# Kernel optimization log

Measured on AMD Instinct MI355X. Metric: run time of the kernel, lower is better.

Reference implementation:

```python
import jax, jax.numpy as jnp
import numpy as np
from jax import lax

T, B, C = 16, 16, 256          # TIMESTEPS, BATCH_SIZE, corr channels
HS, HT = 31, 15                 # search / target feature spatial; VALID corr -> 17x17
OUT = HS - HT + 1               # 17


def setup_inputs() -> dict:
    key = jax.random.key(0)
    k1, k2, k3 = jax.random.split(key, 3)
    s_f = jax.random.normal(k1, (T * B, C, HS, HS), dtype=jnp.float32)
    t_f = jax.random.normal(k2, (B, C, HT, HT), dtype=jnp.float32)
    pos_list = jax.random.randint(k3, (B, T, 2), 0, OUT, dtype=jnp.int32)
    return {"s_f": s_f, "t_f": t_f, "pos_list": pos_list}


def _depthwise_corr(s_b, t_b):
    # s_b: (T, C, 31, 31) search feats for one batch element across timesteps
    # t_b: (C, 15, 15) its target kernel; depthwise cross-correlation per channel
    k = t_b[:, None]  # (C, 1, 15, 15) OIHW with O=C, I=1
    return lax.conv_general_dilated(
        s_b, k, window_strides=(1, 1), padding='VALID',
        dimension_numbers=('NCHW', 'OIHW', 'NCHW'),
        feature_group_count=C)  # (T, C, 17, 17)


def reference(s_f, t_f, pos_list):
    # Correlation_func: torch loops over T doing grouped conv2d; fused here.
    s = s_f.reshape(T, B, C, HS, HS).transpose(1, 0, 2, 3, 4)  # (B, T, C, 31, 31)
    corr = jax.vmap(_depthwise_corr)(s, t_f)                   # (B, T, C, 17, 17)
    # forward(): corr_feat.reshape(T,B,256,17,17).permute(1,0,3,4,2) -> (B,T,17,17,C)
    feat = corr.transpose(0, 1, 3, 4, 2)
    # Chiose_RoW: nested per-element gather -> single advanced-index gather
    bi = jnp.arange(B)[:, None]   # (B, 1)
    ti = jnp.arange(T)[None, :]   # (1, T)
    masks_feat = feat[bi, ti, pos_list[..., 0], pos_list[..., 1]]  # (B, T, C)
    return corr, masks_feat
```

## Files before the change

### kernel.cpp

```cpp
#include <hip/hip_runtime.h>
#include <stdint.h>

#define TT 16
#define BB 16
#define CC 256
#define HS 31
#define HT 15
#define OUTW 17
#define NCH 15
#define NCHAN (BB*TT*CC)
#define CORR_ELEMS ((size_t)NCHAN*OUTW*OUTW)
#define SROW 20
#define SCH  620

typedef _Float16 h2_t __attribute__((ext_vector_type(2)));

__device__ __forceinline__ unsigned packh2(float a, float b) {
    return __builtin_bit_cast(unsigned, __builtin_amdgcn_cvt_pkrtz(a, b));
}
__device__ __forceinline__ float fdot2f(unsigned a, unsigned b, float c) {
    return __builtin_amdgcn_fdot2(__builtin_bit_cast(h2_t, a),
                                  __builtin_bit_cast(h2_t, b), c, false);
}

__device__ __forceinline__ int s_index(int ch) {
    int bt = ch >> 8, c = ch & 255;
    int b = bt >> 4, t = bt & 15;
    return (t * BB + b) * CC + c;
}

__global__ __launch_bounds__(256, 1)
void corr_kernel(const float* __restrict__ s_f, const float* __restrict__ t_f,
                 const int* __restrict__ pos,
                 float* __restrict__ corr, float* __restrict__ masks)
{
    __shared__ unsigned lds[NCH * SCH];

    const int tid = threadIdx.x;
    const int ch_base = blockIdx.x * NCH;

    {
        const int jcol = tid & 15;
        const int r0   = tid >> 4;
        const int x0   = 2 * jcol;
        const bool hasb  = (jcol < 15);
        const int  r1    = r0 + 16;
        const bool hasr1 = (r1 <= 30);
        const int xa = hasb ? x0 : x0 - 1;

        float2 La[NCH], Lb[NCH];
#pragma unroll
        for (int j = 0; j < NCH; ++j) {
            int ch = ch_base + j; if (ch >= NCHAN) ch = NCHAN - 1;
            const float* src = s_f + (size_t)s_index(ch) * (HS * HS);
            La[j] = *(const float2*)(src + r0 * HS + xa);
            Lb[j] = hasr1 ? *(const float2*)(src + r1 * HS + xa)
                          : make_float2(0.f, 0.f);
        }
#pragma unroll
        for (int j = 0; j < NCH; ++j) {
            float a0 = hasb ? La[j].x : La[j].y;
            float b0 = hasb ? La[j].y : 0.0f;
            lds[j * SCH + r0 * SROW + jcol] = packh2(a0, b0);
            if (hasr1) {
                float a1 = hasb ? Lb[j].x : Lb[j].y;
                float b1 = hasb ? Lb[j].y : 0.0f;
                lds[j * SCH + r1 * SROW + jcol] = packh2(a1, b1);
            }
        }
    }

    {
        float2 Lw[8];
        int    off[8];
#pragma unroll
        for (int it = 0; it < 8; ++it) {
            int idx = tid + 256 * it;
            bool ok = idx < NCH * HT * 8;
            int i2  = ok ? idx : 0;
            int j   = i2 / (HT * 8);
            int e   = i2 - j * (HT * 8);
            int ky  = e >> 3, p = e & 7;
            int ch  = ch_base + j; if (ch >= NCHAN) ch = NCHAN - 1;
            int bt = ch >> 8, c = ch & 255, b = bt >> 4;
            const float* wsrc = t_f + (size_t)(b * CC + c) * (HT * HT) + ky * HT;
            int xw = (p < 7) ? 2 * p : 13;
            Lw[it] = *(const float2*)(wsrc + xw);
            off[it] = ok ? (j * SCH + 40 * ky + 16 + ((p & 4) ? 20 + (p & 3) : (p & 3)))
                         : -1;
            if (p == 7) { Lw[it].x = Lw[it].y; Lw[it].y = 0.0f; }
        }
#pragma unroll
        for (int it = 0; it < 8; ++it)
            if (off[it] >= 0) lds[off[it]] = packh2(Lw[it].x, Lw[it].y);
    }

    __syncthreads();

    const int c_sub = tid / OUTW;
    const int oy    = tid - c_sub * OUTW;
    if (c_sub >= NCH) return;
    const int ch = ch_base + c_sub;
    if (ch >= NCHAN) return;

    const unsigned* chb = lds + c_sub * SCH;

    float acc[OUTW];
#pragma unroll
    for (int m = 0; m < OUTW; ++m) acc[m] = 0.0f;

    uint4 A0, A1, A2, A3, AW0, AW1;
    uint4 B0, B1, B2, B3, BW0, BW1;

#define LOADS(S0,S1,S2,S3,W0,W1,KY) do {                                   \
        const uint4* sr = (const uint4*)(chb + (oy + (KY)) * SROW);        \
        S0 = sr[0]; S1 = sr[1]; S2 = sr[2]; S3 = sr[3];                    \
        W0 = *(const uint4*)(chb + 40 * (KY) + 16);                        \
        W1 = *(const uint4*)(chb + 40 * (KY) + 36);                        \
    } while (0)

#define COMPUTE(S0,S1,S2,S3,W0,W1) do {                                    \
        unsigned sp[16] = {S0.x,S0.y,S0.z,S0.w, S1.x,S1.y,S1.z,S1.w,       \
                           S2.x,S2.y,S2.z,S2.w, S3.x,S3.y,S3.z,S3.w};      \
        unsigned wp[8]  = {W0.x,W0.y,W0.z,W0.w, W1.x,W1.y,W1.z,W1.w};      \
        unsigned wo_[8];                                                   \
        wo_[0] = wp[0] << 16;                                              \
        _Pragma("unroll")                                                  \
        for (int r = 1; r < 8; ++r)                                        \
            wo_[r] = __builtin_amdgcn_alignbit(wp[r], wp[r - 1], 16);      \
        _Pragma("unroll")                                                  \
        for (int e = 0; e < 9; ++e)                                        \
            _Pragma("unroll")                                              \
            for (int jj = 0; jj < 8; ++jj)                                 \
                acc[2 * e] = fdot2f(sp[e + jj], wp[jj], acc[2 * e]);       \
        _Pragma("unroll")                                                  \
        for (int o = 0; o < 8; ++o)                                        \
            _Pragma("unroll")                                              \
            for (int r = 0; r < 8; ++r)                                    \
                acc[2 * o + 1] = fdot2f(sp[o + r], wo_[r], acc[2 * o + 1]);\
    } while (0)

    LOADS(A0,A1,A2,A3,AW0,AW1, 0);
#pragma unroll 1
    for (int kk = 0; kk < 7; ++kk) {
        LOADS(B0,B1,B2,B3,BW0,BW1, 2 * kk + 1);
        COMPUTE(A0,A1,A2,A3,AW0,AW1);
        LOADS(A0,A1,A2,A3,AW0,AW1, 2 * kk + 2);
        COMPUTE(B0,B1,B2,B3,BW0,BW1);
    }
    COMPUTE(A0,A1,A2,A3,AW0,AW1);

#undef LOADS
#undef COMPUTE

    float* outp = corr + (size_t)ch * (OUTW * OUTW) + (size_t)oy * OUTW;
#pragma unroll
    for (int m = 0; m < OUTW; ++m) outp[m] = acc[m];

    const int bt = ch >> 8;
    const int p0 = pos[2 * bt];
    const int p1 = pos[2 * bt + 1];
    if (oy == p0) {
        float v = acc[0];
#pragma unroll
        for (int m = 1; m < OUTW; ++m) v = (p1 == m) ? acc[m] : v;
        masks[ch] = v;
    }
}

extern "C" void kernel_launch(void* const* d_in, const int* in_sizes, int n_in,
                              void* d_out, int out_size, void* d_ws, size_t ws_size,
                              hipStream_t stream)
{
    const float* s_f = (const float*)d_in[0];
    const float* t_f = (const float*)d_in[1];
    const int*   pos = (const int*)d_in[2];
    float* corr  = (float*)d_out;
    float* masks = corr + CORR_ELEMS;

    int nblocks = (NCHAN + NCH - 1) / NCH;
    corr_kernel<<<nblocks, 256, 0, stream>>>(s_f, t_f, pos, corr, masks);
}
```

Baseline: 124.8 us.

## Switch correlation from packed fp16 dot2 to fp32 FMA with swizzled LDS

Stores search and target tiles in LDS as fp32 instead of packed fp16 pairs, and computes the depthwise correlation with plain fp32 FMAs rather than fdot2. Search rows use an XOR swizzle on float4 columns to avoid bank conflicts. Channels per block drop from 15 to 13 and the launch bound allows 2 blocks per CU to fit the larger LDS footprint. This removes fp16 rounding error, but it roughly doubles the FMA instruction count and the LDS traffic.

```diff
diff --git a/kernel.cpp b/kernel.cpp
--- a/kernel.cpp
+++ b/kernel.cpp
@@ -7,21 +7,13 @@
 #define HS 31
 #define HT 15
 #define OUTW 17
-#define NCH 15
+#define NCH 13
 #define NCHAN (BB*TT*CC)
 #define CORR_ELEMS ((size_t)NCHAN*OUTW*OUTW)
-#define SROW 20
-#define SCH  620
-
-typedef _Float16 h2_t __attribute__((ext_vector_type(2)));
-
-__device__ __forceinline__ unsigned packh2(float a, float b) {
-    return __builtin_bit_cast(unsigned, __builtin_amdgcn_cvt_pkrtz(a, b));
-}
-__device__ __forceinline__ float fdot2f(unsigned a, unsigned b, float c) {
-    return __builtin_amdgcn_fdot2(__builtin_bit_cast(h2_t, a),
-                                  __builtin_bit_cast(h2_t, b), c, false);
-}
+#define SROW 32
+#define SOFF 992
+#define WROW 16
+#define SCH  1236
 
 __device__ __forceinline__ int s_index(int ch) {
     int bt = ch >> 8, c = ch & 255;
@@ -29,12 +21,12 @@
     return (t * BB + b) * CC + c;
 }
 
-__global__ __launch_bounds__(256, 1)
+__global__ __launch_bounds__(256, 2)
 void corr_kernel(const float* __restrict__ s_f, const float* __restrict__ t_f,
                  const int* __restrict__ pos,
                  float* __restrict__ corr, float* __restrict__ masks)
 {
-    __shared__ unsigned lds[NCH * SCH];
+    __shared__ float lds[NCH * SCH];
 
     const int tid = threadIdx.x;
     const int ch_base = blockIdx.x * NCH;
@@ -57,15 +49,27 @@
             Lb[j] = hasr1 ? *(const float2*)(src + r1 * HS + xa)
                           : make_float2(0.f, 0.f);
         }
+        const int u0 = jcol >> 1;
+        const int lo = x0 & 3;
 #pragma unroll
         for (int j = 0; j < NCH; ++j) {
-            float a0 = hasb ? La[j].x : La[j].y;
-            float b0 = hasb ? La[j].y : 0.0f;
-            lds[j * SCH + r0 * SROW + jcol] = packh2(a0, b0);
+            {
+                int col = (((u0) ^ (r0 & 7)) << 2) | lo;
+                if (hasb) {
+                    *(float2*)&lds[j * SCH + r0 * SROW + col] = La[j];
+                } else {
+                    int c30 = ((7 ^ (r0 & 7)) << 2) | 2;
+                    lds[j * SCH + r0 * SROW + c30] = La[j].y;
+                }
+            }
             if (hasr1) {
-                float a1 = hasb ? Lb[j].x : Lb[j].y;
-                float b1 = hasb ? Lb[j].y : 0.0f;
-                lds[j * SCH + r1 * SROW + jcol] = packh2(a1, b1);
+                if (hasb) {
+                    int col = (((u0) ^ (r1 & 7)) << 2) | lo;
+                    *(float2*)&lds[j * SCH + r1 * SROW + col] = Lb[j];
+                } else {
+                    int c30 = ((7 ^ (r1 & 7)) << 2) | 2;
+                    lds[j * SCH + r1 * SROW + c30] = Lb[j].y;
+                }
             }
         }
     }
@@ -86,13 +90,12 @@
             const float* wsrc = t_f + (size_t)(b * CC + c) * (HT * HT) + ky * HT;
             int xw = (p < 7) ? 2 * p : 13;
             Lw[it] = *(const float2*)(wsrc + xw);
-            off[it] = ok ? (j * SCH + 40 * ky + 16 + ((p & 4) ? 20 + (p & 3) : (p & 3)))
-                         : -1;
             if (p == 7) { Lw[it].x = Lw[it].y; Lw[it].y = 0.0f; }
+            off[it] = ok ? (j * SCH + SOFF + ky * WROW + 2 * p) : -1;
         }
 #pragma unroll
         for (int it = 0; it < 8; ++it)
-            if (off[it] >= 0) lds[off[it]] = packh2(Lw[it].x, Lw[it].y);
+            if (off[it] >= 0) *(float2*)&lds[off[it]] = Lw[it];
     }
 
     __syncthreads();
@@ -103,55 +106,41 @@
     const int ch = ch_base + c_sub;
     if (ch >= NCHAN) return;
 
-    const unsigned* chb = lds + c_sub * SCH;
+    const float* chb = lds + c_sub * SCH;
 
     float acc[OUTW];
 #pragma unroll
     for (int m = 0; m < OUTW; ++m) acc[m] = 0.0f;
 
-    uint4 A0, A1, A2, A3, AW0, AW1;
-    uint4 B0, B1, B2, B3, BW0, BW1;
+#pragma unroll 1
+    for (int ky = 0; ky < HT; ++ky) {
+        const int y  = oy + ky;
+        const int yb = y & 7;
+        const float4* srow = (const float4*)(chb + y * SROW);
 
-#define LOADS(S0,S1,S2,S3,W0,W1,KY) do {                                   \
-        const uint4* sr = (const uint4*)(chb + (oy + (KY)) * SROW);        \
-        S0 = sr[0]; S1 = sr[1]; S2 = sr[2]; S3 = sr[3];                    \
-        W0 = *(const uint4*)(chb + 40 * (KY) + 16);                        \
-        W1 = *(const uint4*)(chb + 40 * (KY) + 36);                        \
-    } while (0)
+        float sv[32];
+#pragma unroll
+        for (int u = 0; u < 8; ++u) {
+            float4 d = srow[u ^ yb];
+            sv[4 * u + 0] = d.x; sv[4 * u + 1] = d.y;
+            sv[4 * u + 2] = d.z; sv[4 * u + 3] = d.w;
+        }
 
-#define COMPUTE(S0,S1,S2,S3,W0,W1) do {                                    \
-        unsigned sp[16] = {S0.x,S0.y,S0.z,S0.w, S1.x,S1.y,S1.z,S1.w,       \
-                           S2.x,S2.y,S2.z,S2.w, S3.x,S3.y,S3.z,S3.w};      \
-        unsigned wp[8]  = {W0.x,W0.y,W0.z,W0.w, W1.x,W1.y,W1.z,W1.w};      \
-        unsigned wo_[8];                                                   \
-        wo_[0] = wp[0] << 16;                                              \
-        _Pragma("unroll")                                                  \
-        for (int r = 1; r < 8; ++r)                                        \
-            wo_[r] = __builtin_amdgcn_alignbit(wp[r], wp[r - 1], 16);      \
-        _Pragma("unroll")                                                  \
-        for (int e = 0; e < 9; ++e)                                        \
-            _Pragma("unroll")                                              \
-            for (int jj = 0; jj < 8; ++jj)                                 \
-                acc[2 * e] = fdot2f(sp[e + jj], wp[jj], acc[2 * e]);       \
-        _Pragma("unroll")                                                  \
-        for (int o = 0; o < 8; ++o)                                        \
-            _Pragma("unroll")                                              \
-            for (int r = 0; r < 8; ++r)                                    \
-                acc[2 * o + 1] = fdot2f(sp[o + r], wo_[r], acc[2 * o + 1]);\
-    } while (0)
+        const float4* wr = (const float4*)(chb + SOFF + ky * WROW);
+        float wv[16];
+#pragma unroll
+        for (int u = 0; u < 4; ++u) {
+            float4 d = wr[u];
+            wv[4 * u + 0] = d.x; wv[4 * u + 1] = d.y;
+            wv[4 * u + 2] = d.z; wv[4 * u + 3] = d.w;
+        }
 
-    LOADS(A0,A1,A2,A3,AW0,AW1, 0);
-#pragma unroll 1
-    for (int kk = 0; kk < 7; ++kk) {
-        LOADS(B0,B1,B2,B3,BW0,BW1, 2 * kk + 1);
-        COMPUTE(A0,A1,A2,A3,AW0,AW1);
-        LOADS(A0,A1,A2,A3,AW0,AW1, 2 * kk + 2);
-        COMPUTE(B0,B1,B2,B3,BW0,BW1);
+#pragma unroll
+        for (int kx = 0; kx < HT; ++kx)
+#pragma unroll
+            for (int m = 0; m < OUTW; ++m)
+                acc[m] = fmaf(sv[m + kx], wv[kx], acc[m]);
     }
-    COMPUTE(A0,A1,A2,A3,AW0,AW1);
-
-#undef LOADS
-#undef COMPUTE
 
     float* outp = corr + (size_t)ch * (OUTW * OUTW) + (size_t)oy * OUTW;
 #pragma unroll
```

Result: slower. 179.8 us (median of 4 runs) (+44.1%).
